# Kernel tuning notes

Hardware: AMD Instinct MI355X
Metric: run time of the kernel (lower is better)

Reference implementation:

```python
import jax, jax.numpy as jnp
import numpy as np


def conv1x1(x, W, b):
    # 1x1 Conv2d == per-pixel linear over channels. x: [B,C,H,W], W: [O,C], b: [O]
    return jnp.einsum('oc,bchw->bohw', W, x) + b[None, :, None, None]


def setup_inputs() -> dict:
    key = jax.random.key(0)
    ks = jax.random.split(key, 18)
    B, C, Hd, H, W = 16, 64, 64, 32, 32
    s = 0.05
    f = jax.random.normal
    return {
        'h': f(ks[0], (B, C, H, W), jnp.float32),
        'm': f(ks[1], (B, C, H, W), jnp.float32),
        'Wq': f(ks[2], (Hd, C), jnp.float32) * s,
        'bq': f(ks[3], (Hd,), jnp.float32) * s,
        'Wk': f(ks[4], (Hd, C), jnp.float32) * s,
        'bk': f(ks[5], (Hd,), jnp.float32) * s,
        'Wk2': f(ks[6], (Hd, C), jnp.float32) * s,
        'bk2': f(ks[7], (Hd,), jnp.float32) * s,
        'Wv': f(ks[8], (C, C), jnp.float32) * s,
        'bv': f(ks[9], (C,), jnp.float32) * s,
        'Wv2': f(ks[10], (C, C), jnp.float32) * s,
        'bv2': f(ks[11], (C,), jnp.float32) * s,
        'Wz': f(ks[12], (2 * C, 2 * C), jnp.float32) * s,
        'bz': f(ks[13], (2 * C,), jnp.float32) * s,
        'Wm': f(ks[14], (3 * C, 3 * C), jnp.float32) * s,
        'bm': f(ks[15], (3 * C,), jnp.float32) * s,
    }


def reference(h, m, Wq, bq, Wk, bk, Wk2, bk2, Wv, bv, Wv2, bv2, Wz, bz, Wm, bm):
    B, C, H, W = h.shape
    Hd = Wq.shape[0]
    N = H * W
    # Shared query from h
    Q_h = conv1x1(h, Wq, bq).reshape(B, Hd, N).transpose(0, 2, 1)  # [B,N,Hd]
    # Self-attention branch over h
    K_h = conv1x1(h, Wk, bk).reshape(B, Hd, N)                     # [B,Hd,N]
    A_h = jax.nn.softmax(jnp.einsum('bnd,bdm->bnm', Q_h, K_h), axis=-1)  # [B,N,N]
    V_h = conv1x1(h, Wv, bv).reshape(B, C, N)                      # [B,C,N]
    Z_h = jnp.einsum('bnm,bcm->bcn', A_h, V_h).reshape(B, C, H, W)
    # Cross-attention branch over memory m (same query Q_h)
    K_m = conv1x1(m, Wk2, bk2).reshape(B, Hd, N)
    A_m = jax.nn.softmax(jnp.einsum('bnd,bdm->bnm', Q_h, K_m), axis=-1)
    V_m = conv1x1(m, Wv2, bv2).reshape(B, C, N)
    Z_m = jnp.einsum('bnm,bcm->bcn', A_m, V_m).reshape(B, C, H, W)
    # Fuse and gated memory update
    Z = conv1x1(jnp.concatenate([Z_h, Z_m], axis=1), Wz, bz)       # [B,2C,H,W]
    combined = conv1x1(jnp.concatenate([Z, h], axis=1), Wm, bm)    # [B,3C,H,W]
    mo, mg, mi = combined[:, :C], combined[:, C:2 * C], combined[:, 2 * C:]
    mi = jax.nn.sigmoid(mi)
    new_m = (1 - mi) * m + mi * jnp.tanh(mg)
    new_h = jax.nn.sigmoid(mo) * new_m
    return (new_h, new_m)
```

## Files before the change

kernel.cpp:

```cpp
#include <hip/hip_runtime.h>

typedef unsigned short u16;
typedef unsigned int u32;
typedef __attribute__((ext_vector_type(8))) short bf16x8;
typedef __attribute__((ext_vector_type(4))) short bf16x4;
typedef __attribute__((ext_vector_type(4))) float f32x4;

#define MFMA(a, b, c) __builtin_amdgcn_mfma_f32_16x16x32_bf16((a), (b), (c), 0, 0, 0)
#define MFMA16(a, b, c) __builtin_amdgcn_mfma_f32_16x16x16bf16_1k((a), (b), (c), 0, 0, 0)

static __device__ __forceinline__ u16 f2bf(float x) {
  u32 u = __float_as_uint(x);
  u += 0x7FFFu + ((u >> 16) & 1u);
  return (u16)(u >> 16);
}
static __device__ __forceinline__ u32 packbf_t(float hi, float lo) {
  return __builtin_amdgcn_perm(__float_as_uint(hi), __float_as_uint(lo), 0x07060302u);
}
static __device__ __forceinline__ u32 packbf(float lo, float hi) {
  return (u32)f2bf(lo) | ((u32)f2bf(hi) << 16);
}

__global__ __launch_bounds__(256) void proj_kernel(
    const float* __restrict__ h, const float* __restrict__ m_,
    const float* __restrict__ bq, const float* __restrict__ bk,
    const float* __restrict__ bk2, const float* __restrict__ bv,
    const float* __restrict__ bv2,
    const float* __restrict__ Wq, const float* __restrict__ Wk,
    const float* __restrict__ Wk2, const float* __restrict__ Wv,
    const float* __restrict__ Wv2,
    const float* __restrict__ Wz, const float* __restrict__ Wm,
    const float* __restrict__ bm,
    u16* __restrict__ Qb, u16* __restrict__ Khb, u16* __restrict__ Kmb,
    u16* __restrict__ Vhb, u16* __restrict__ Vmb, u16* __restrict__ hbuf,
    u16* __restrict__ Wzb, u16* __restrict__ Wmb, float* __restrict__ bmp)
{
  const int tid = threadIdx.x;
  const int b = blockIdx.y, n0 = blockIdx.x * 64, z = blockIdx.z;

  {
    const int gid = (blockIdx.z * 256 + blockIdx.y * 16 + blockIdx.x) * 256 + tid;
    if (gid < 16384) {
      Wzb[gid] = f2bf(Wz[gid]);
    } else if (gid < 53248) {
      const int e = gid - 16384;
      const int p = e / 192, k = e % 192;
      const int hb2 = p / 96, r1 = p % 96, ctl = r1 / 48, r2 = r1 % 48;
      const int g = r2 >> 4, mm = r2 & 15;
      const int o = g * 64 + (hb2 * 2 + ctl) * 16 + mm;
      Wmb[p * 192 + k] = f2bf(Wm[o * 192 + k]);
    } else if (gid < 53440) {
      const int p = gid - 53248;
      const int hb2 = p / 96, r1 = p % 96, ctl = r1 / 48, r2 = r1 % 48;
      const int g = r2 >> 4, mm = r2 & 15;
      const int o = g * 64 + (hb2 * 2 + ctl) * 16 + mm;
      bmp[p] = bm[o];
    }
  }

  __shared__ __align__(16) u16 xt[64][72];
  const float* __restrict__ X = (z >= 3) ? m_ : h;

  {
    const int px = tid & 63, c0 = (tid >> 6) * 16;
#pragma unroll
    for (int i = 0; i < 8; ++i) {
      const int c = c0 + 2 * i;
      const float f0 = X[(b * 64 + c) * 1024 + n0 + px];
      const float f1 = X[(b * 64 + c + 1) * 1024 + n0 + px];
      *(u32*)&xt[px][c] = packbf(f0, f1);
    }
  }
  __syncthreads();

  const int lane = tid & 63, w = tid >> 6;
  const int mm = lane & 15, q = lane >> 4;

  const bf16x8 xa0 = *(const bf16x8*)&xt[w * 16 + mm][q * 8];
  const bf16x8 xa1 = *(const bf16x8*)&xt[w * 16 + mm][32 + q * 8];

  auto ldw8 = [&](const float* Wf, int row, int col0) {
    const float4 a = *(const float4*)(Wf + row * 64 + col0);
    const float4 bb = *(const float4*)(Wf + row * 64 + col0 + 4);
    union { u32 u[4]; bf16x8 v; } r;
    r.u[0] = packbf(a.x, a.y);
    r.u[1] = packbf(a.z, a.w);
    r.u[2] = packbf(bb.x, bb.y);
    r.u[3] = packbf(bb.z, bb.w);
    return r.v;
  };

  auto qk_store = [&](u16* dst, const float* Wf, const float* bias) {
#pragma unroll
    for (int ot = 0; ot < 4; ++ot) {
      const bf16x8 wb0 = ldw8(Wf, ot * 16 + mm, q * 8);
      const bf16x8 wb1 = ldw8(Wf, ot * 16 + mm, 32 + q * 8);
      const float4 b4 = *(const float4*)(bias + ot * 16 + q * 4);
      f32x4 d = {b4.x, b4.y, b4.z, b4.w};
      d = MFMA(wb0, xa0, d);
      d = MFMA(wb1, xa1, d);
      uint2 val;
      val.x = packbf(d[0], d[1]);
      val.y = packbf(d[2], d[3]);
      *(uint2*)(dst + (b * 1024 + n0 + w * 16 + mm) * 64 + ot * 16 + q * 4) = val;
    }
  };
  auto v_store = [&](u16* dst, const float* Wf, const float* bias) {
#pragma unroll
    for (int ot = 0; ot < 4; ++ot) {
      const bf16x8 wb0 = ldw8(Wf, ot * 16 + mm, q * 8);
      const bf16x8 wb1 = ldw8(Wf, ot * 16 + mm, 32 + q * 8);
      const float bb = bias[ot * 16 + mm];
      f32x4 d = {bb, bb, bb, bb};
      d = MFMA(xa0, wb0, d);
      d = MFMA(xa1, wb1, d);
      uint2 val;
      val.x = packbf(d[0], d[1]);
      val.y = packbf(d[2], d[3]);
      *(uint2*)(dst + b * 65536 + blockIdx.x * 4096 + w * 1024 +
                (ot * 16 + mm) * 16 + q * 4) = val;
    }
  };

  if (z == 0) {
    qk_store(Qb, Wq, bq);
    const int px = tid >> 2, sg = tid & 3;
    u32* dst = (u32*)(hbuf + (b * 1024 + n0 + px) * 64 + sg * 16);
    const u16* srcr = &xt[px][sg * 16];
#pragma unroll
    for (int j = 0; j < 8; ++j) dst[j] = *(const u32*)(srcr + 2 * j);
  } else if (z == 1) {
    qk_store(Khb, Wk, bk);
  } else if (z == 2) {
    v_store(Vhb, Wv, bv);
  } else if (z == 3) {
    qk_store(Kmb, Wk2, bk2);
  } else {
    v_store(Vmb, Wv2, bv2);
  }
}

__global__ __launch_bounds__(256) void attn_tail_kernel(
    const u16* __restrict__ Qb, const u16* __restrict__ Khb,
    const u16* __restrict__ Kmb, const u16* __restrict__ Vhb,
    const u16* __restrict__ Vmb, const u16* __restrict__ hbuf,
    const float* __restrict__ m_, const u16* __restrict__ Wzb,
    const float* __restrict__ bz, const u16* __restrict__ Wmb,
    const float* __restrict__ bmp, float* __restrict__ out)
{
  const int id = blockIdx.x;
  const int b = id & 15;
  const int qg = id >> 4;
  const int q0 = qg * 32;

  const u16* __restrict__ Kh = Khb + b * 65536;
  const u16* __restrict__ Vh = Vhb + b * 65536;
  const u16* __restrict__ Km = Kmb + b * 65536;
  const u16* __restrict__ Vm = Vmb + b * 65536;

  __shared__ __align__(16) u16 pool[21504];
  __shared__ __align__(16) u16 zp[32][136];
  __shared__ float rsw[4][32];

  const int tid = threadIdx.x, w = tid >> 6, lane = tid & 63;
  const int mm = lane & 15, q = lane >> 4;

  u16* const warena = pool + w * 5376;

  bf16x8 qb0[2], qb1[2];
#pragma unroll
  for (int qt = 0; qt < 2; ++qt) {
    const u16* Qp = Qb + (b * 1024 + q0 + qt * 16 + mm) * 64;
    qb0[qt] = *(const bf16x8*)(Qp + q * 8);
    qb1[qt] = *(const bf16x8*)(Qp + 32 + q * 8);
  }

  f32x4 zA[2][4], zB[2][4];
  float rpA[2] = {0.f, 0.f}, rpB[2] = {0.f, 0.f};
#pragma unroll
  for (int qt = 0; qt < 2; ++qt)
#pragma unroll
    for (int ct = 0; ct < 4; ++ct) {
      zA[qt][ct] = (f32x4){0.f, 0.f, 0.f, 0.f};
      zB[qt][ct] = (f32x4){0.f, 0.f, 0.f, 0.f};
    }

  uint4 k0, k1, v0, v1;
  auto ldg = [&](const u16* K, const u16* V, int kc) {
    const u16* Ks = K + kc * 4096 + w * 1024 + lane * 16;
    const u16* Vs = V + kc * 4096 + w * 1024 + lane * 16;
    k0 = *(const uint4*)Ks;
    k1 = *(const uint4*)(Ks + 8);
    v0 = *(const uint4*)Vs;
    v1 = *(const uint4*)(Vs + 8);
  };
  auto stl = [&](int buf) {
    u16* Kd = warena + buf * 2688 + (lane >> 2) * 72 + (lane & 3) * 16;
    u16* Vd = warena + buf * 2688 + 1152 + lane * 24;
    *(uint4*)Kd = k0;
    *(uint4*)(Kd + 8) = k1;
    *(uint4*)Vd = v0;
    *(uint4*)(Vd + 8) = v1;
  };

  auto compute = [&](int buf, f32x4 (&z)[2][4], float (&rp)[2]) {
    const u16* Kt = warena + buf * 2688;
    const u16* Vt = warena + buf * 2688 + 1152;
    const bf16x8 kf0 = *(const bf16x8*)(Kt + mm * 72 + q * 8);
    const bf16x8 kf1 = *(const bf16x8*)(Kt + mm * 72 + 32 + q * 8);
    bf16x4 vf[4];
#pragma unroll
    for (int ct = 0; ct < 4; ++ct)
      vf[ct] = *(const bf16x4*)(Vt + (ct * 16 + mm) * 24 + q * 4);

#pragma unroll
    for (int qt = 0; qt < 2; ++qt) {
      f32x4 s = {0.f, 0.f, 0.f, 0.f};
      s = MFMA(kf0, qb0[qt], s);
      s = MFMA(kf1, qb1[qt], s);
      const float e0 = __expf(s[0]), e1 = __expf(s[1]);
      const float e2 = __expf(s[2]), e3 = __expf(s[3]);
      rp[qt] += (e0 + e1) + (e2 + e3);
      union { u32 u[2]; bf16x4 v; } pb;
      pb.u[0] = packbf_t(e1, e0);
      pb.u[1] = packbf_t(e3, e2);
#pragma unroll
      for (int ct = 0; ct < 4; ++ct) z[qt][ct] = MFMA16(vf[ct], pb.v, z[qt][ct]);
    }
  };

  auto attn_pass = [&](const u16* K, const u16* V, f32x4 (&z)[2][4],
                       float (&rp)[2]) {
    ldg(K, V, 0);
    stl(0);
    ldg(K, V, 1);
    int cur = 0;
#pragma unroll 1
    for (int kc = 0; kc < 16; ++kc) {
      compute(cur, z, rp);
      if (kc < 15) {
        stl(cur ^ 1);
        if (kc < 14) ldg(K, V, kc + 2);
        cur ^= 1;
      }
    }
  };

  attn_pass(Kh, Vh, zA, rpA);
  attn_pass(Km, Vm, zB, rpB);

  __syncthreads();

  u16* const zcb = pool;
  auto combine = [&](int br, f32x4 (&z)[2][4], float (&rp)[2]) {
#pragma unroll
    for (int qt = 0; qt < 2; ++qt) {
      float v = rp[qt];
      v += __shfl_xor(v, 16);
      v += __shfl_xor(v, 32);
      if (q == 0) rsw[w][qt * 16 + mm] = v;
#pragma unroll
      for (int ct = 0; ct < 4; ++ct) {
        uint2 val;
        val.x = packbf_t(z[qt][ct][1], z[qt][ct][0]);
        val.y = packbf_t(z[qt][ct][3], z[qt][ct][2]);
        *(uint2*)(zcb + w * 2176 + (qt * 16 + mm) * 68 + ct * 16 + q * 4) = val;
      }
    }
    __syncthreads();
    const int c2 = tid & 31, qr = tid >> 5;
#pragma unroll
    for (int i = 0; i < 4; ++i) {
      const int query = qr + i * 8;
      const float rt = rsw[0][query] + rsw[1][query] + rsw[2][query] + rsw[3][query];
      const float rinv = __builtin_amdgcn_rcpf(rt);
      float vlo = 0.f, vhi = 0.f;
#pragma unroll
      for (int ww = 0; ww < 4; ++ww) {
        const u32 u = *(const u32*)(zcb + ww * 2176 + query * 68 + c2 * 2);
        vlo += __uint_as_float(u << 16);
        vhi += __uint_as_float(u & 0xffff0000u);
      }
      vlo *= rinv;
      vhi *= rinv;
      *(u32*)&zp[query][br * 64 + c2 * 2] = packbf_t(vhi, vlo);
    }
    __syncthreads();
  };
  combine(0, zA, rpA);
  combine(1, zB, rpB);

  const int pxt = w & 1, oh = w >> 1;
  u16* const zp2 = pool;
  {
    bf16x8 za[4];
#pragma unroll
    for (int ks = 0; ks < 4; ++ks)
      za[ks] = *(const bf16x8*)&zp[pxt * 16 + mm][ks * 32 + q * 8];
#pragma unroll
    for (int ot = 0; ot < 4; ++ot) {
      const int o0 = oh * 64 + ot * 16;
      const float4 b4 = *(const float4*)(bz + o0 + q * 4);
      f32x4 d = {b4.x, b4.y, b4.z, b4.w};
#pragma unroll
      for (int ks = 0; ks < 4; ++ks) {
        const bf16x8 wb = *(const bf16x8*)(Wzb + (o0 + mm) * 128 + ks * 32 + q * 8);
        d = MFMA(wb, za[ks], d);
      }
      uint2 val;
      val.x = packbf(d[0], d[1]);
      val.y = packbf(d[2], d[3]);
      *(uint2*)(zp2 + (pxt * 16 + mm) * 136 + o0 + q * 4) = val;
    }
  }
  __syncthreads();

  {
    const int hb2 = oh;
    bf16x8 fa[6];
#pragma unroll
    for (int ks = 0; ks < 4; ++ks)
      fa[ks] = *(const bf16x8*)(zp2 + (pxt * 16 + mm) * 136 + ks * 32 + q * 8);
    {
      const u16* hp = hbuf + (b * 1024 + q0 + pxt * 16 + mm) * 64;
      fa[4] = *(const bf16x8*)(hp + q * 8);
      fa[5] = *(const bf16x8*)(hp + 32 + q * 8);
    }
    f32x4 dd[6];
#pragma unroll
    for (int j = 0; j < 6; ++j) {
      const int p = hb2 * 96 + j * 16 + mm;
      const float bb = bmp[p];
      f32x4 d = {bb, bb, bb, bb};
#pragma unroll
      for (int ks = 0; ks < 6; ++ks) {
        const bf16x8 wb = *(const bf16x8*)(Wmb + p * 192 + ks * 32 + q * 8);
        d = MFMA(fa[ks], wb, d);
      }
      dd[j] = d;
    }
#pragma unroll
    for (int ctl = 0; ctl < 2; ++ctl) {
      const int c = (hb2 * 2 + ctl) * 16 + mm;
      const int px = q0 + pxt * 16 + q * 4;
      const float4 mold = *(const float4*)(m_ + (b * 64 + c) * 1024 + px);
      float4 nh, nm;
#pragma unroll
      for (int r = 0; r < 4; ++r) {
        const float xo = dd[ctl * 3 + 0][r];
        const float xg = dd[ctl * 3 + 1][r];
        const float xi = dd[ctl * 3 + 2][r];
        const float si = __builtin_amdgcn_rcpf(1.f + __expf(-xi));
        const float th = 1.f - 2.f * __builtin_amdgcn_rcpf(__expf(2.f * xg) + 1.f);
        const float so = __builtin_amdgcn_rcpf(1.f + __expf(-xo));
        const float mo = ((const float*)&mold)[r];
        const float nmv = (1.f - si) * mo + si * th;
        ((float*)&nm)[r] = nmv;
        ((float*)&nh)[r] = so * nmv;
      }
      *(float4*)(out + (b * 64 + c) * 1024 + px) = nh;
      *(float4*)(out + 1048576 + (b * 64 + c) * 1024 + px) = nm;
    }
  }
}

extern "C" void kernel_launch(void* const* d_in, const int* in_sizes, int n_in,
                              void* d_out, int out_size, void* d_ws, size_t ws_size,
                              hipStream_t stream) {
  const float* h   = (const float*)d_in[0];
  const float* m   = (const float*)d_in[1];
  const float* Wq  = (const float*)d_in[2];
  const float* bq  = (const float*)d_in[3];
  const float* Wk  = (const float*)d_in[4];
  const float* bk  = (const float*)d_in[5];
  const float* Wk2 = (const float*)d_in[6];
  const float* bk2 = (const float*)d_in[7];
  const float* Wv  = (const float*)d_in[8];
  const float* bv  = (const float*)d_in[9];
  const float* Wv2 = (const float*)d_in[10];
  const float* bv2 = (const float*)d_in[11];
  const float* Wz  = (const float*)d_in[12];
  const float* bz  = (const float*)d_in[13];
  const float* Wm  = (const float*)d_in[14];
  const float* bm  = (const float*)d_in[15];
  float* out = (float*)d_out;

  char* ws = (char*)d_ws;
  const size_t MB = 1024 * 1024;
  u16* Qb   = (u16*)(ws + 0 * MB);
  u16* Khb  = (u16*)(ws + 2 * MB);
  u16* Kmb  = (u16*)(ws + 4 * MB);
  u16* Vhb  = (u16*)(ws + 6 * MB);
  u16* Vmb  = (u16*)(ws + 8 * MB);
  u16* hbuf = (u16*)(ws + 10 * MB);
  u16* Wzb  = (u16*)(ws + 16 * MB + 40960);
  u16* Wmb  = (u16*)(ws + 16 * MB + 73728);
  float* bmp = (float*)(ws + 16 * MB + 147456);

  proj_kernel<<<dim3(16, 16, 5), 256, 0, stream>>>(
      h, m, bq, bk, bk2, bv, bv2, Wq, Wk, Wk2, Wv, Wv2, Wz, Wm, bm,
      Qb, Khb, Kmb, Vhb, Vmb, hbuf, Wzb, Wmb, bmp);
  attn_tail_kernel<<<512, 256, 0, stream>>>(Qb, Khb, Kmb, Vhb, Vmb, hbuf, m,
                                            Wzb, bz, Wmb, bmp, out);
}
```

Before: 138.5 us.

## Interleave self and cross attention passes in a single key-chunk loop

The two sequential attention passes over h and m are merged into one loop that handles a chunk of each branch per iteration. Each branch now gets its own single LDS buffer instead of a double buffer, and keeps its own prefetch registers loaded two chunks ahead. The goal is to expose two independent MFMA, exp and load chains per iteration to hide latency and cut loop overhead. The cost is more live registers for the second set of prefetch data, which could lower occupancy. Each branch also writes its LDS slot right after reading it within the same wave.

```diff
diff --git a/kernel.cpp b/kernel.cpp
--- a/kernel.cpp
+++ b/kernel.cpp
@@ -165,7 +165,8 @@
   const int tid = threadIdx.x, w = tid >> 6, lane = tid & 63;
   const int mm = lane & 15, q = lane >> 4;
 
-  u16* const warena = pool + w * 5376;
+  u16* const arenaH = pool + w * 5376;
+  u16* const arenaM = arenaH + 2688;
 
   bf16x8 qb0[2], qb1[2];
 #pragma unroll
@@ -185,27 +186,29 @@
       zB[qt][ct] = (f32x4){0.f, 0.f, 0.f, 0.f};
     }
 
-  uint4 k0, k1, v0, v1;
-  auto ldg = [&](const u16* K, const u16* V, int kc) {
+  uint4 kh0, kh1, vh0, vh1, km0, km1, vm0, vm1;
+  auto ldg = [&](const u16* K, const u16* V, int kc, uint4& r0, uint4& r1,
+                 uint4& s0, uint4& s1) {
     const u16* Ks = K + kc * 4096 + w * 1024 + lane * 16;
     const u16* Vs = V + kc * 4096 + w * 1024 + lane * 16;
-    k0 = *(const uint4*)Ks;
-    k1 = *(const uint4*)(Ks + 8);
-    v0 = *(const uint4*)Vs;
-    v1 = *(const uint4*)(Vs + 8);
-  };
-  auto stl = [&](int buf) {
-    u16* Kd = warena + buf * 2688 + (lane >> 2) * 72 + (lane & 3) * 16;
-    u16* Vd = warena + buf * 2688 + 1152 + lane * 24;
-    *(uint4*)Kd = k0;
-    *(uint4*)(Kd + 8) = k1;
-    *(uint4*)Vd = v0;
-    *(uint4*)(Vd + 8) = v1;
-  };
-
-  auto compute = [&](int buf, f32x4 (&z)[2][4], float (&rp)[2]) {
-    const u16* Kt = warena + buf * 2688;
-    const u16* Vt = warena + buf * 2688 + 1152;
+    r0 = *(const uint4*)Ks;
+    r1 = *(const uint4*)(Ks + 8);
+    s0 = *(const uint4*)Vs;
+    s1 = *(const uint4*)(Vs + 8);
+  };
+  auto stl = [&](u16* arena, const uint4& r0, const uint4& r1, const uint4& s0,
+                 const uint4& s1) {
+    u16* Kd = arena + (lane >> 2) * 72 + (lane & 3) * 16;
+    u16* Vd = arena + 1152 + lane * 24;
+    *(uint4*)Kd = r0;
+    *(uint4*)(Kd + 8) = r1;
+    *(uint4*)Vd = s0;
+    *(uint4*)(Vd + 8) = s1;
+  };
+
+  auto compute = [&](const u16* arena, f32x4 (&z)[2][4], float (&rp)[2]) {
+    const u16* Kt = arena;
+    const u16* Vt = arena + 1152;
     const bf16x8 kf0 = *(const bf16x8*)(Kt + mm * 72 + q * 8);
     const bf16x8 kf1 = *(const bf16x8*)(Kt + mm * 72 + 32 + q * 8);
     bf16x4 vf[4];
@@ -229,25 +232,26 @@
     }
   };
 
-  auto attn_pass = [&](const u16* K, const u16* V, f32x4 (&z)[2][4],
-                       float (&rp)[2]) {
-    ldg(K, V, 0);
-    stl(0);
-    ldg(K, V, 1);
-    int cur = 0;
+  ldg(Kh, Vh, 0, kh0, kh1, vh0, vh1);
+  stl(arenaH, kh0, kh1, vh0, vh1);
+  ldg(Km, Vm, 0, km0, km1, vm0, vm1);
+  stl(arenaM, km0, km1, vm0, vm1);
+  ldg(Kh, Vh, 1, kh0, kh1, vh0, vh1);
+  ldg(Km, Vm, 1, km0, km1, vm0, vm1);
+
 #pragma unroll 1
-    for (int kc = 0; kc < 16; ++kc) {
-      compute(cur, z, rp);
-      if (kc < 15) {
-        stl(cur ^ 1);
-        if (kc < 14) ldg(K, V, kc + 2);
-        cur ^= 1;
-      }
-    }
-  };
-
-  attn_pass(Kh, Vh, zA, rpA);
-  attn_pass(Km, Vm, zB, rpB);
+  for (int kc = 0; kc < 16; ++kc) {
+    compute(arenaH, zA, rpA);
+    if (kc < 15) {
+      stl(arenaH, kh0, kh1, vh0, vh1);
+      if (kc < 14) ldg(Kh, Vh, kc + 2, kh0, kh1, vh0, vh1);
+    }
+    compute(arenaM, zB, rpB);
+    if (kc < 15) {
+      stl(arenaM, km0, km1, vm0, vm1);
+      if (kc < 14) ldg(Km, Vm, kc + 2, km0, km1, vm0, vm1);
+    }
+  }
 
   __syncthreads();
 
```

Result: faster. 133.5 us (median of 2 runs) (-3.6%).
